# Optimization experiments

Hardware: AMD Instinct MI355X
Metric: run time of the kernel (lower is better)

The kernel has to match this reference:

```python
import jax, jax.numpy as jnp
import numpy as np

TEMP1 = 4.0  # self.temp1

def l2norm(x, eps=1e-8):
    # matches torch ref: x / (sqrt(sum(x^2)) + eps)
    return x / (jnp.sqrt(jnp.sum(x * x, axis=-1, keepdims=True)) + eps)

def setup_inputs() -> dict:
    key = jax.random.key(0)
    ks = jax.random.split(key, 8)
    B, C, H, W, D, Q = 32, 1024, 16, 16, 1000, 64
    return {
        "img_features_l": jax.random.normal(ks[0], (B, C, H, W), jnp.float32),
        "img_features_f": jax.random.normal(ks[1], (B, C, H, W), jnp.float32),
        "words_emb": jax.random.normal(ks[2], (B, D, Q), jnp.float32),
        "conv_w": jax.random.normal(ks[3], (D, C), jnp.float32) * 0.02,
        "conv_b": jnp.zeros((D,), jnp.float32),
        "sa_wl": jax.random.normal(ks[4], (D, D), jnp.float32) * 0.02,
        "sa_bl": jnp.zeros((D,), jnp.float32),
        "sa_wg": jax.random.normal(ks[5], (D, D), jnp.float32) * 0.02,
        "sa_bg": jnp.zeros((D,), jnp.float32),
        "sa_wc": jax.random.normal(ks[6], (D,), jnp.float32) * 0.05,
        "sa_bc": jnp.zeros((), jnp.float32),
        "cap_w": jax.random.normal(ks[7], (D,), jnp.float32) * 0.05,
        "cap_b": jnp.zeros((), jnp.float32),
    }

def reference(img_features_l, img_features_f, words_emb, conv_w, conv_b,
              sa_wl, sa_bl, sa_wg, sa_bg, sa_wc, sa_bc, cap_w, cap_b):
    B = img_features_f.shape[0]
    Bw = words_emb.shape[0]
    # 1x1 conv (1024 -> 1000), then flatten spatial and concat frontal+lateral
    f = jnp.einsum('oc,bchw->bohw', conv_w, img_features_f) + conv_b[None, :, None, None]
    l = jnp.einsum('oc,bchw->bohw', conv_w, img_features_l) + conv_b[None, :, None, None]
    img = jnp.concatenate([f.reshape(B, f.shape[1], -1),
                           l.reshape(B, l.shape[1], -1)], axis=2)  # [B, D, S]

    # attention_fn, vectorized over the per-word Python loop (axis i)
    # attn[i,b,s,q] = sum_d img[b,d,s] * words[i,d,q]
    logits = jnp.einsum('bds,idq->ibsq', img, words_emb)            # [Bw,B,S,Q]
    a1 = jax.nn.softmax(logits, axis=-1)                            # softmax over queryL
    a2 = jax.nn.softmax(jnp.swapaxes(a1, -1, -2) * TEMP1, axis=-1)  # [Bw,B,Q,S], softmax over sourceL
    # weightedContext (already transposed to [i,b,q,d])
    wctx = jnp.einsum('bds,ibqs->ibqd', img, a2)                    # [Bw,B,Q,D]

    word_t = jnp.swapaxes(words_emb, 1, 2)[:, None]                 # [Bw,1,Q,D]
    sim_loc = l2norm(wctx * word_t)                                 # [Bw,B,Q,D]
    sim_ave = jnp.mean(sim_loc, axis=2)                             # [Bw,B,D]

    # SA module (dropout in eval mode => identity)
    l_emb = jnp.tanh(jnp.einsum('ibqd,de->ibqe', sim_loc, sa_wl) + sa_bl)
    g_emb = jnp.tanh(jnp.einsum('ibd,de->ibe', sim_ave, sa_wg) + sa_bg)
    common = l_emb * g_emb[:, :, None, :]                           # [Bw,B,Q,D]
    w = jnp.einsum('ibqd,d->ibq', common, sa_wc) + sa_bc            # [Bw,B,Q]
    w = jax.nn.softmax(w, axis=-1)
    new_global = l2norm(jnp.einsum('ibq,ibqd->ibd', w, sim_loc))    # [Bw,B,D]
    sim = jax.nn.sigmoid(jnp.einsum('ibd,d->ib', new_global, cap_w) + cap_b)

    similarities_cap = sim.T                                        # [B, Bw]
    att_maps = a2[jnp.arange(Bw), jnp.arange(Bw)]                   # [Bw,Q,S] (attn[i] per word i)
    return similarities_cap, att_maps
```

## Files before the change

kernel.cpp:

```cpp
#include <hip/hip_runtime.h>
#include <cstdint>

typedef unsigned short u16;
typedef unsigned int   u32;
typedef __attribute__((ext_vector_type(8))) short bf16x8;
typedef __attribute__((ext_vector_type(4))) float f32x4;

#define D_DIM 1000
#define C_IN  1024
#define HW    256
#define S_DIM 512
#define Q_DIM 64

__device__ __forceinline__ u16 f2b(float x) {
    u32 u = __builtin_bit_cast(u32, x);
    u32 r = (u + 0x7FFFu + ((u >> 16) & 1u)) >> 16;
    return (u16)r;
}
__device__ __forceinline__ float b2f(u16 h) {
    u32 u = ((u32)h) << 16;
    return __builtin_bit_cast(float, u);
}
__device__ __forceinline__ float ftanh(float x) {
    float e = __expf(2.f * x);
    return 1.f - 2.f / (e + 1.f);
}

#define GLOAD(ldsptr, gptr) \
    __builtin_amdgcn_global_load_lds( \
        (const __attribute__((address_space(1))) unsigned int*)(gptr), \
        (__attribute__((address_space(3))) unsigned int*)(ldsptr), 16, 0, 0)

__global__ __launch_bounds__(256) void k_prepAll(
    const float* __restrict__ feat_l, const float* __restrict__ feat_f,
    const float* __restrict__ cw, const float* __restrict__ words,
    const float* __restrict__ wl,
    u16* __restrict__ fT_hi, u16* __restrict__ fT_lo,
    u16* __restrict__ cwh, u16* __restrict__ cwl,
    u16* __restrict__ wth, u16* __restrict__ wtl,
    u16* __restrict__ wlT)
{
    __shared__ char SH[18432] __attribute__((aligned(16)));
    const int bid = blockIdx.x;
    const int tid = threadIdx.x;

    if (bid < 4096) {
        float (*T)[65] = (float(*)[65])SH;
        int ct = bid & 15, ht = (bid >> 4) & 3, half_ = (bid >> 6) & 1, b = bid >> 7;
        const float* src = (half_ ? feat_l : feat_f) + (size_t)b * C_IN * HW;
        {
            int cl = tid >> 2, h16 = (tid & 3) * 16;
            const float* p = src + (size_t)(ct * 64 + cl) * 256 + ht * 64 + h16;
            #pragma unroll
            for (int j = 0; j < 4; j++) {
                float4 v = *(const float4*)(p + j * 4);
                T[h16 + j * 4 + 0][cl] = v.x;
                T[h16 + j * 4 + 1][cl] = v.y;
                T[h16 + j * 4 + 2][cl] = v.z;
                T[h16 + j * 4 + 3][cl] = v.w;
            }
        }
        __syncthreads();
        {
            int hl = tid >> 2, c16 = (tid & 3) * 16;
            int srow = b * 512 + half_ * 256 + ht * 64 + hl;
            bf16x8 vh[2], vlo[2];
            #pragma unroll
            for (int g = 0; g < 2; g++)
                #pragma unroll
                for (int j = 0; j < 8; j++) {
                    float x = T[hl][c16 + g * 8 + j];
                    u16 hh = f2b(x);
                    vh[g][j] = (short)hh;
                    vlo[g][j] = (short)f2b(x - b2f(hh));
                }
            size_t o = (size_t)srow * 1024 + ct * 64 + c16;
            *(bf16x8*)(fT_hi + o) = vh[0];
            *(bf16x8*)(fT_hi + o + 8) = vh[1];
            *(bf16x8*)(fT_lo + o) = vlo[0];
            *(bf16x8*)(fT_lo + o + 8) = vlo[1];
        }
    } else if (bid < 5120) {
        int d = bid - 4096;
        int c4 = tid * 4;
        ushort4 h = make_ushort4(0, 0, 0, 0), lo = make_ushort4(0, 0, 0, 0);
        if (d < D_DIM) {
            float4 v = *(const float4*)(cw + (size_t)d * 1024 + c4);
            float a[4] = {v.x, v.y, v.z, v.w};
            u16* ph = (u16*)&h; u16* pl = (u16*)&lo;
            #pragma unroll
            for (int j = 0; j < 4; j++) {
                ph[j] = f2b(a[j]);
                pl[j] = f2b(a[j] - b2f(ph[j]));
            }
        }
        *(ushort4*)(cwh + (size_t)d * 1024 + c4) = h;
        *(ushort4*)(cwl + (size_t)d * 1024 + c4) = lo;
    } else if (bid < 5632) {
        int lb = bid - 5120;
        int i = lb >> 4, dt = lb & 15;
        const float* src = words + (size_t)i * D_DIM * Q_DIM;
        u16 (*Th)[72] = (u16(*)[72])SH;
        u16 (*Tl)[72] = (u16(*)[72])(SH + 9216);
        #pragma unroll
        for (int rep = 0; rep < 4; rep++) {
            int idx = tid + rep * 256;
            int dl = idx >> 4, q4 = (idx & 15) * 4;
            int d = dt * 64 + dl;
            float4 v = make_float4(0.f, 0.f, 0.f, 0.f);
            if (d < D_DIM) v = *(const float4*)(src + (size_t)d * Q_DIM + q4);
            float a[4] = {v.x, v.y, v.z, v.w};
            #pragma unroll
            for (int jj = 0; jj < 4; jj++) {
                u16 hh = f2b(a[jj]);
                Th[dl][q4 + jj] = hh;
                Tl[dl][q4 + jj] = f2b(a[jj] - b2f(hh));
            }
        }
        __syncthreads();
        #pragma unroll
        for (int rep = 0; rep < 2; rep++) {
            int idx = tid + rep * 256;
            int q = idx >> 3, c8 = idx & 7;
            bf16x8 vh, vlo;
            #pragma unroll
            for (int jj = 0; jj < 8; jj++) { vh[jj] = (short)Th[c8 * 8 + jj][q]; vlo[jj] = (short)Tl[c8 * 8 + jj][q]; }
            size_t doff = (size_t)i * 65536 + (size_t)q * 1024 + dt * 64 + c8 * 8;
            *(bf16x8*)(wth + doff) = vh;
            *(bf16x8*)(wtl + doff) = vlo;
        }
    } else {
        int lb = bid - 5632;
        float (*t)[65] = (float(*)[65])SH;
        int bd = lb & 15, be = lb >> 4;
        int tx = tid & 15, ty = tid >> 4;
        #pragma unroll
        for (int rr = 0; rr < 4; rr++) {
            int r = ty * 4 + rr;
            int d = bd * 64 + r;
            int e4 = be * 64 + tx * 4;
            float v0 = 0.f, v1 = 0.f, v2 = 0.f, v3 = 0.f;
            if (d < D_DIM) {
                if (e4 + 3 < D_DIM) {
                    float4 v = *reinterpret_cast<const float4*>(wl + (size_t)d * D_DIM + e4);
                    v0 = v.x; v1 = v.y; v2 = v.z; v3 = v.w;
                } else {
                    if (e4 + 0 < D_DIM) v0 = wl[(size_t)d * D_DIM + e4 + 0];
                    if (e4 + 1 < D_DIM) v1 = wl[(size_t)d * D_DIM + e4 + 1];
                    if (e4 + 2 < D_DIM) v2 = wl[(size_t)d * D_DIM + e4 + 2];
                    if (e4 + 3 < D_DIM) v3 = wl[(size_t)d * D_DIM + e4 + 3];
                }
            }
            t[r][tx * 4 + 0] = v0; t[r][tx * 4 + 1] = v1;
            t[r][tx * 4 + 2] = v2; t[r][tx * 4 + 3] = v3;
        }
        __syncthreads();
        #pragma unroll
        for (int rr = 0; rr < 4; rr++) {
            int r2 = ty * 4 + rr;
            int e = be * 64 + r2;
            int d0 = bd * 64 + tx * 4;
            ushort4 h;
            h.x = f2b(t[tx * 4 + 0][r2]); h.y = f2b(t[tx * 4 + 1][r2]);
            h.z = f2b(t[tx * 4 + 2][r2]); h.w = f2b(t[tx * 4 + 3][r2]);
            *reinterpret_cast<ushort4*>(wlT + (size_t)e * 1024 + d0) = h;
        }
    }
}

__global__ __launch_bounds__(512) void k_convG(
    const u16* __restrict__ fT_hi, const u16* __restrict__ fT_lo,
    const u16* __restrict__ cwh, const u16* __restrict__ cwl,
    const float* __restrict__ cb,
    u16* __restrict__ img_hi, u16* __restrict__ imgT_hi, u16* __restrict__ imgT_lo)
{
    const int bid0 = blockIdx.x;
    const int bid = (bid0 & 7) * 32 + (bid0 >> 3);
    const int mblk = bid >> 2, nt = bid & 3;
    const int m0 = mblk * 256, n0 = nt * 256;

    __shared__ char LDS[131072] __attribute__((aligned(16)));
    __shared__ float cbS[256];

    const int tid = threadIdx.x;
    const int wid = tid >> 6, lane = tid & 63;
    const int wr = wid >> 2, wc = wid & 3;
    const int l15 = lane & 15, l4 = lane >> 4;
    const int sw = (l15 >> 1) & 3;

    if (tid < 256) {
        int d = n0 + tid;
        cbS[tid] = (d < D_DIM) ? cb[d] : 0.f;
    }

    auto stage = [&](int buf, int k0) {
        char* base = LDS + buf * 65536;
        #pragma unroll
        for (int rep = 0; rep < 2; rep++) {
            int idx = tid + rep * 512;
            int row = idx >> 2, slot = idx & 3;
            int kb = (slot ^ ((row >> 1) & 3)) * 16;
            size_t ao = (size_t)(m0 + row) * 2048 + (size_t)k0 * 2 + kb;
            size_t bo = (size_t)(n0 + row) * 2048 + (size_t)k0 * 2 + kb;
            GLOAD(base + idx * 16, (const char*)fT_hi + ao);
            GLOAD(base + 16384 + idx * 16, (const char*)fT_lo + ao);
            GLOAD(base + 32768 + idx * 16, (const char*)cwh + bo);
            GLOAD(base + 49152 + idx * 16, (const char*)cwl + bo);
        }
    };

    f32x4 acc[8][4] = {};

    stage(0, 0);
    __syncthreads();
    int cur = 0;
    for (int k0 = 0; k0 < 1024; k0 += 32) {
        if (k0 + 32 < 1024) stage(cur ^ 1, k0 + 32);
        const char* Ah = LDS + cur * 65536;
        const char* Alo = Ah + 16384;
        const char* Bh = Ah + 32768;
        const char* Blo = Ah + 49152;
        bf16x8 ah[8], bh[4];
        #pragma unroll
        for (int mf = 0; mf < 8; mf++)
            ah[mf] = *(const bf16x8*)(Ah + (wr * 128 + mf * 16 + l15) * 64 + ((l4 ^ sw) * 16));
        #pragma unroll
        for (int nf = 0; nf < 4; nf++)
            bh[nf] = *(const bf16x8*)(Bh + (wc * 64 + nf * 16 + l15) * 64 + ((l4 ^ sw) * 16));
        #pragma unroll
        for (int mf = 0; mf < 8; mf++)
            #pragma unroll
            for (int nf = 0; nf < 4; nf++)
                acc[mf][nf] = __builtin_amdgcn_mfma_f32_16x16x32_bf16(ah[mf], bh[nf], acc[mf][nf], 0, 0, 0);
        #pragma unroll
        for (int mf = 0; mf < 8; mf++) {
            bf16x8 al = *(const bf16x8*)(Alo + (wr * 128 + mf * 16 + l15) * 64 + ((l4 ^ sw) * 16));
            #pragma unroll
            for (int nf = 0; nf < 4; nf++)
                acc[mf][nf] = __builtin_amdgcn_mfma_f32_16x16x32_bf16(al, bh[nf], acc[mf][nf], 0, 0, 0);
        }
        #pragma unroll
        for (int nf = 0; nf < 4; nf++) {
            bf16x8 bl = *(const bf16x8*)(Blo + (wc * 64 + nf * 16 + l15) * 64 + ((l4 ^ sw) * 16));
            #pragma unroll
            for (int mf = 0; mf < 8; mf++)
                acc[mf][nf] = __builtin_amdgcn_mfma_f32_16x16x32_bf16(ah[mf], bl, acc[mf][nf], 0, 0, 0);
        }
        __syncthreads();
        cur ^= 1;
    }
    const int b = m0 >> 9;
    const int sbase = m0 & 511;
    #pragma unroll
    for (int mf = 0; mf < 8; mf++) {
        int srow = sbase + wr * 128 + mf * 16 + l4 * 4;
        #pragma unroll
        for (int nf = 0; nf < 4; nf++) {
            int dcol = n0 + wc * 64 + nf * 16 + l15;
            float bias = cbS[wc * 64 + nf * 16 + l15];
            ushort4 h4;
            u16* ph = (u16*)&h4;
            #pragma unroll
            for (int r = 0; r < 4; r++)
                ph[r] = f2b(acc[mf][nf][r] + bias);
            *(ushort4*)(img_hi + ((size_t)b * 1024 + dcol) * 512 + srow) = h4;
        }
    }
    u16* Thi = (u16*)LDS;
    u16* Tlo = (u16*)(LDS + 33792);
    #pragma unroll
    for (int qt = 0; qt < 4; qt++) {
        __syncthreads();
        if (wr == (qt >> 1)) {
            #pragma unroll
            for (int mm = 0; mm < 4; mm++) {
                int mf = (qt & 1) * 4 + mm;
                int sq = mm * 16 + l4 * 4;
                #pragma unroll
                for (int nf = 0; nf < 4; nf++) {
                    int dcol = wc * 64 + nf * 16 + l15;
                    float bias = cbS[dcol];
                    #pragma unroll
                    for (int r = 0; r < 4; r++) {
                        float v = acc[mf][nf][r] + bias;
                        u16 hh = f2b(v);
                        Thi[(sq + r) * 264 + dcol] = hh;
                        Tlo[(sq + r) * 264 + dcol] = f2b(v - b2f(hh));
                    }
                }
            }
        }
        __syncthreads();
        #pragma unroll
        for (int rep = 0; rep < 4; rep++) {
            int g = tid + rep * 512;
            int s = g >> 5, d8 = (g & 31) * 8;
            size_t go = ((size_t)b * 512 + sbase + qt * 64 + s) * 1024 + n0 + d8;
            *(bf16x8*)(imgT_hi + go) = *(const bf16x8*)(&Thi[s * 264 + d8]);
            *(bf16x8*)(imgT_lo + go) = *(const bf16x8*)(&Tlo[s * 264 + d8]);
        }
    }
}

__global__ __launch_bounds__(512) void k_logits(
    const u16* __restrict__ wTh, const u16* __restrict__ wTl,
    const u16* __restrict__ iTh, const u16* __restrict__ iTl,
    u16* __restrict__ U, float* __restrict__ Zp, float* __restrict__ out)
{
    const int bid0 = blockIdx.x;
    const int bid = (bid0 & 7) * 64 + (bid0 >> 3);
    const int b = bid >> 4, mt = (bid >> 1) & 7, nt = bid & 1;
    const int m0 = mt * 256, n0 = nt * 256;

    __shared__ char LDS[131072] __attribute__((aligned(16)));

    const int tid = threadIdx.x;
    const int wid = tid >> 6, lane = tid & 63;
    const int wr = wid >> 2, wc = wid & 3;
    const int l15 = lane & 15, l4 = lane >> 4;
    const int sw = (l15 >> 1) & 3;

    auto stage = [&](int buf, int k0) {
        char* base = LDS + buf * 65536;
        #pragma unroll
        for (int rep = 0; rep < 2; rep++) {
            int idx = tid + rep * 512;
            int row = idx >> 2, slot = idx & 3;
            int kb = (slot ^ ((row >> 1) & 3)) * 16;
            size_t ao = (size_t)(m0 + row) * 2048 + (size_t)k0 * 2 + kb;
            size_t bo = ((size_t)b * 512 + n0 + row) * 2048 + (size_t)k0 * 2 + kb;
            GLOAD(base + idx * 16, (const char*)wTh + ao);
            GLOAD(base + 16384 + idx * 16, (const char*)wTl + ao);
            GLOAD(base + 32768 + idx * 16, (const char*)iTh + bo);
            GLOAD(base + 49152 + idx * 16, (const char*)iTl + bo);
        }
    };

    f32x4 acc[8][4] = {};

    stage(0, 0);
    __syncthreads();
    int cur = 0;
    for (int k0 = 0; k0 < 1024; k0 += 32) {
        if (k0 + 32 < 1024) stage(cur ^ 1, k0 + 32);
        const char* Ah = LDS + cur * 65536;
        const char* Alo = Ah + 16384;
        const char* Bh = Ah + 32768;
        const char* Blo = Ah + 49152;
        bf16x8 ah[8], bh[4];
        #pragma unroll
        for (int mf = 0; mf < 8; mf++)
            ah[mf] = *(const bf16x8*)(Ah + (wr * 128 + mf * 16 + l15) * 64 + ((l4 ^ sw) * 16));
        #pragma unroll
        for (int nf = 0; nf < 4; nf++)
            bh[nf] = *(const bf16x8*)(Bh + (wc * 64 + nf * 16 + l15) * 64 + ((l4 ^ sw) * 16));
        #pragma unroll
        for (int mf = 0; mf < 8; mf++)
            #pragma unroll
            for (int nf = 0; nf < 4; nf++)
                acc[mf][nf] = __builtin_amdgcn_mfma_f32_16x16x32_bf16(ah[mf], bh[nf], acc[mf][nf], 0, 0, 0);
        #pragma unroll
        for (int mf = 0; mf < 8; mf++) {
            bf16x8 al = *(const bf16x8*)(Alo + (wr * 128 + mf * 16 + l15) * 64 + ((l4 ^ sw) * 16));
            #pragma unroll
            for (int nf = 0; nf < 4; nf++)
                acc[mf][nf] = __builtin_amdgcn_mfma_f32_16x16x32_bf16(al, bh[nf], acc[mf][nf], 0, 0, 0);
        }
        #pragma unroll
        for (int nf = 0; nf < 4; nf++) {
            bf16x8 bl = *(const bf16x8*)(Blo + (wc * 64 + nf * 16 + l15) * 64 + ((l4 ^ sw) * 16));
            #pragma unroll
            for (int mf = 0; mf < 8; mf++)
                acc[mf][nf] = __builtin_amdgcn_mfma_f32_16x16x32_bf16(ah[mf], bl, acc[mf][nf], 0, 0, 0);
        }
        __syncthreads();
        cur ^= 1;
    }

    float zacc[8][4] = {};
    #pragma unroll
    for (int il = 0; il < 2; il++) {
        int i_glob = mt * 4 + wr * 2 + il;
        bool diag = (i_glob == b);
        #pragma unroll
        for (int nf = 0; nf < 4; nf++) {
            int scol = n0 + wc * 64 + nf * 16 + l15;
            float m = -3.4e38f;
            #pragma unroll
            for (int mm = 0; mm < 4; mm++)
                #pragma unroll
                for (int r = 0; r < 4; r++)
                    m = fmaxf(m, acc[il * 4 + mm][nf][r]);
            m = fmaxf(m, __shfl_xor(m, 16));
            m = fmaxf(m, __shfl_xor(m, 32));
            float e[16], sum = 0.f;
            #pragma unroll
            for (int mm = 0; mm < 4; mm++)
                #pragma unroll
                for (int r = 0; r < 4; r++) {
                    float ev = __expf(acc[il * 4 + mm][nf][r] - m);
                    e[mm * 4 + r] = ev; sum += ev;
                }
            sum += __shfl_xor(sum, 16);
            sum += __shfl_xor(sum, 32);
            float inv = 1.f / sum;
            #pragma unroll
            for (int mm = 0; mm < 4; mm++)
                #pragma unroll
                for (int r = 0; r < 4; r++) {
                    float u = __expf(4.f * e[mm * 4 + r] * inv);
                    u16 ub = f2b(u);
                    zacc[il * 4 + mm][r] += b2f(ub);
                    int iqrow = m0 + wr * 128 + (il * 4 + mm) * 16 + l4 * 4 + r;
                    U[((size_t)b * 2048 + iqrow) * 512 + scol] = ub;
                    if (diag) {
                        int q = iqrow & 63;
                        out[1024 + ((size_t)i_glob * 64 + q) * 512 + scol] = u;
                    }
                }
        }
    }
    #pragma unroll
    for (int mf = 0; mf < 8; mf++)
        #pragma unroll
        for (int r = 0; r < 4; r++) {
            float z = zacc[mf][r];
            z += __shfl_xor(z, 1); z += __shfl_xor(z, 2);
            z += __shfl_xor(z, 4); z += __shfl_xor(z, 8);
            if (l15 == 0) {
                int iqrow = m0 + wr * 128 + mf * 16 + l4 * 4 + r;
                Zp[((size_t)b * 2048 + iqrow) * 8 + nt * 4 + wc] = z;
            }
        }
}

__global__ __launch_bounds__(256) void k_zat(
    const float* __restrict__ Zp, float* __restrict__ invZf, float* __restrict__ out)
{
    const int bid = blockIdx.x;
    const int tid = threadIdx.x;
    if (bid < 256) {
        int gi = bid * 256 + tid;
        float4 z0 = *(const float4*)(Zp + (size_t)gi * 8);
        float4 z1 = *(const float4*)(Zp + (size_t)gi * 8 + 4);
        invZf[gi] = 1.f / (z0.x + z0.y + z0.z + z0.w + z1.x + z1.y + z1.z + z1.w);
    } else {
        const int i = bid - 256;
        float* am = out + 1024 + (size_t)i * Q_DIM * S_DIM;
        int q = tid >> 2, ch = tid & 3;
        float s = 0.f;
        for (int ss = ch * 128; ss < ch * 128 + 128; ss++) s += am[(size_t)q * S_DIM + ss];
        s += __shfl_xor(s, 1);
        s += __shfl_xor(s, 2);
        float iz = 1.f / s;
        for (int ss = ch * 128; ss < ch * 128 + 128; ss++) am[(size_t)q * S_DIM + ss] *= iz;
    }
}

__global__ __launch_bounds__(512) void k_wctx(
    const u16* __restrict__ img_hi, const u16* __restrict__ U,
    const float* __restrict__ invZf,
    const u16* __restrict__ wTh, const u16* __restrict__ wTl,
    u16* __restrict__ vbuf, float* __restrict__ ssqp)
{
    const int bid0 = blockIdx.x;
    const int bid = (bid0 & 7) * 128 + (bid0 >> 3);
    const int b = bid >> 5, mt = (bid >> 3) & 3, nt = bid & 7;
    const int m0 = mt * 256, n0 = nt * 256;

    __shared__ char LDS[65536] __attribute__((aligned(16)));
    __shared__ float izS[256];

    const int tid = threadIdx.x;
    const int wid = tid >> 6, lane = tid & 63;
    const int wr = wid >> 2, wc = wid & 3;
    const int l15 = lane & 15, l4 = lane >> 4;
    const int sw = (l15 >> 1) & 3;

    if (tid < 256) izS[tid] = invZf[b * 2048 + n0 + tid];

    auto stage = [&](int buf, int k0) {
        char* base = LDS + buf * 32768;
        #pragma unroll
        for (int rep = 0; rep < 2; rep++) {
            int idx = tid + rep * 512;
            int row = idx >> 2, slot = idx & 3;
            int kb = (slot ^ ((row >> 1) & 3)) * 16;
            GLOAD(base + idx * 16, (const char*)img_hi + ((size_t)b * 1024 + m0 + row) * 1024 + (size_t)k0 * 2 + kb);
            GLOAD(base + 16384 + idx * 16, (const char*)U + ((size_t)b * 2048 + n0 + row) * 1024 + (size_t)k0 * 2 + kb);
        }
    };

    f32x4 acc[8][4] = {};

    stage(0, 0);
    __syncthreads();
    int cur = 0;
    for (int k0 = 0; k0 < 512; k0 += 32) {
        if (k0 + 32 < 512) stage(cur ^ 1, k0 + 32);
        const char* At = LDS + cur * 32768;
        const char* Bt = At + 16384;
        bf16x8 a[8], bb[4];
        #pragma unroll
        for (int mf = 0; mf < 8; mf++)
            a[mf] = *(const bf16x8*)(At + (wr * 128 + mf * 16 + l15) * 64 + ((l4 ^ sw) * 16));
        #pragma unroll
        for (int nf = 0; nf < 4; nf++)
            bb[nf] = *(const bf16x8*)(Bt + (wc * 64 + nf * 16 + l15) * 64 + ((l4 ^ sw) * 16));
        #pragma unroll
        for (int mf = 0; mf < 8; mf++)
            #pragma unroll
            for (int nf = 0; nf < 4; nf++)
                acc[mf][nf] = __builtin_amdgcn_mfma_f32_16x16x32_bf16(a[mf], bb[nf], acc[mf][nf], 0, 0, 0);
        __syncthreads();
        cur ^= 1;
    }

    #pragma unroll
    for (int nf = 0; nf < 4; nf++) {
        int col = wc * 64 + nf * 16 + l15;
        int iq = n0 + col;
        float iz = izS[col];
        size_t wtoff = (size_t)iq * 1024;
        float s_nf = 0.f;
        #pragma unroll
        for (int mf = 0; mf < 8; mf++) {
            int d0 = m0 + wr * 128 + mf * 16 + l4 * 4;
            ushort4 wh = *(const ushort4*)(wTh + wtoff + d0);
            ushort4 wl = *(const ushort4*)(wTl + wtoff + d0);
            const u16* pwh = (const u16*)&wh;
            const u16* pwl = (const u16*)&wl;
            ushort4 vo;
            u16* pv = (u16*)&vo;
            #pragma unroll
            for (int r = 0; r < 4; r++) {
                float wv = b2f(pwh[r]) + b2f(pwl[r]);
                float v = acc[mf][nf][r] * iz * wv;
                s_nf = fmaf(v, v, s_nf);
                pv[r] = f2b(v);
            }
            *(ushort4*)(vbuf + ((size_t)b * 2048 + iq) * 1024 + d0) = vo;
        }
        s_nf += __shfl_xor(s_nf, 16);
        s_nf += __shfl_xor(s_nf, 32);
        if (l4 == 0) ssqp[((size_t)b * 2048 + iq) * 4 + mt] = s_nf;
    }
}

__global__ __launch_bounds__(256) void k_postwg(
    const u16* __restrict__ vbuf, const float* __restrict__ ssqp,
    float* __restrict__ invn_ws, u16* __restrict__ simave_bf,
    const float* __restrict__ wg, u16* __restrict__ wgT)
{
    __shared__ char SH[16640] __attribute__((aligned(16)));
    const int bid = blockIdx.x;
    const int tid = threadIdx.x;

    if (bid < 1024) {
        const int pair = bid;
        float* invnS = (float*)SH;
        if (tid < 64) {
            size_t o = ((size_t)pair * 64 + tid) * 4;
            float s = ssqp[o] + ssqp[o + 1] + ssqp[o + 2] + ssqp[o + 3];
            float n = 1.f / (sqrtf(s) + 1e-8f);
            invnS[tid] = n;
            invn_ws[pair * 64 + tid] = n;
        }
        __syncthreads();
        int d0 = tid * 4;
        ushort4 o4 = make_ushort4(0, 0, 0, 0);
        if (d0 < D_DIM) {
            float a0 = 0.f, a1 = 0.f, a2 = 0.f, a3 = 0.f;
            const u16* vb = vbuf + (size_t)pair * 65536;
            for (int q = 0; q < 64; q++) {
                float n = invnS[q];
                ushort4 v = *(const ushort4*)(vb + q * 1024 + d0);
                a0 = fmaf(b2f(v.x), n, a0); a1 = fmaf(b2f(v.y), n, a1);
                a2 = fmaf(b2f(v.z), n, a2); a3 = fmaf(b2f(v.w), n, a3);
            }
            o4.x = f2b(a0 * (1.f / 64.f)); o4.y = f2b(a1 * (1.f / 64.f));
            o4.z = f2b(a2 * (1.f / 64.f)); o4.w = f2b(a3 * (1.f / 64.f));
        }
        *(ushort4*)(simave_bf + (size_t)pair * 1024 + d0) = o4;
    } else {
        int lb = bid - 1024;
        float (*t)[65] = (float(*)[65])SH;
        int bd = lb & 15, be = lb >> 4;
        int tx = tid & 15, ty = tid >> 4;
        #pragma unroll
        for (int rr = 0; rr < 4; rr++) {
            int r = ty * 4 + rr;
            int d = bd * 64 + r;
            int e4 = be * 64 + tx * 4;
            float v0 = 0.f, v1 = 0.f, v2 = 0.f, v3 = 0.f;
            if (d < D_DIM) {
                if (e4 + 3 < D_DIM) {
                    float4 v = *reinterpret_cast<const float4*>(wg + (size_t)d * D_DIM + e4);
                    v0 = v.x; v1 = v.y; v2 = v.z; v3 = v.w;
                } else {
                    if (e4 + 0 < D_DIM) v0 = wg[(size_t)d * D_DIM + e4 + 0];
                    if (e4 + 1 < D_DIM) v1 = wg[(size_t)d * D_DIM + e4 + 1];
                    if (e4 + 2 < D_DIM) v2 = wg[(size_t)d * D_DIM + e4 + 2];
                    if (e4 + 3 < D_DIM) v3 = wg[(size_t)d * D_DIM + e4 + 3];
                }
            }
            t[r][tx * 4 + 0] = v0; t[r][tx * 4 + 1] = v1;
            t[r][tx * 4 + 2] = v2; t[r][tx * 4 + 3] = v3;
        }
        __syncthreads();
        #pragma unroll
        for (int rr = 0; rr < 4; rr++) {
            int r2 = ty * 4 + rr;
            int e = be * 64 + r2;
            int d0 = bd * 64 + tx * 4;
            ushort4 h;
            h.x = f2b(t[tx * 4 + 0][r2]); h.y = f2b(t[tx * 4 + 1][r2]);
            h.z = f2b(t[tx * 4 + 2][r2]); h.w = f2b(t[tx * 4 + 3][r2]);
            *reinterpret_cast<ushort4*>(wgT + (size_t)e * 1024 + d0) = h;
        }
    }
}

__global__ __launch_bounds__(256) void k_g2M(
    const u16* __restrict__ simave_bf, const u16* __restrict__ wgT,
    const float* __restrict__ bg, const float* __restrict__ wc,
    float* __restrict__ g2)
{
    const int mt = blockIdx.x >> 3, nt = blockIdx.x & 7;
    const int m0 = mt * 128, n0 = nt * 128;

    __shared__ char LDS[65536] __attribute__((aligned(16)));
    __shared__ float bgS[128], wcS[128];

    const int tid = threadIdx.x;
    const int wid = tid >> 6, lane = tid & 63;
    const int wr = wid >> 1, wc_ = wid & 1;
    const int l15 = lane & 15, l4 = lane >> 4;
    const int sw = l15 & 7;

    if (tid < 128) {
        int e = n0 + tid;
        bgS[tid] = (e < D_DIM) ? bg[e] : 0.f;
        wcS[tid] = (e < D_DIM) ? wc[e] : 0.f;
    }

    auto stage = [&](int buf, int k0) {
        char* base = LDS + buf * 32768;
        #pragma unroll
        for (int rep = 0; rep < 4; rep++) {
            int idx = tid + rep * 256;
            int row = idx >> 3, slot = idx & 7;
            int kb = (slot ^ (row & 7)) * 16;
            GLOAD(base + idx * 16, (const char*)simave_bf + (size_t)(m0 + row) * 2048 + (size_t)k0 * 2 + kb);
            GLOAD(base + 16384 + idx * 16, (const char*)wgT + (size_t)(n0 + row) * 2048 + (size_t)k0 * 2 + kb);
        }
    };

    f32x4 acc[4][4] = {};

    stage(0, 0);
    __syncthreads();
    int cur = 0;
    for (int k0 = 0; k0 < 1024; k0 += 64) {
        if (k0 + 64 < 1024) stage(cur ^ 1, k0 + 64);
        const char* Al = LDS + cur * 32768;
        const char* Bl = Al + 16384;
        #pragma unroll
        for (int kf = 0; kf < 2; kf++) {
            bf16x8 a[4], bb[4];
            #pragma unroll
            for (int mf = 0; mf < 4; mf++)
                a[mf] = *(const bf16x8*)(Al + (wr * 64 + mf * 16 + l15) * 128 + (((kf * 4 + l4) ^ sw) * 16));
            #pragma unroll
            for (int nf = 0; nf < 4; nf++)
                bb[nf] = *(const bf16x8*)(Bl + (wc_ * 64 + nf * 16 + l15) * 128 + (((kf * 4 + l4) ^ sw) * 16));
            #pragma unroll
            for (int mf = 0; mf < 4; mf++)
                #pragma unroll
                for (int nf = 0; nf < 4; nf++)
                    acc[mf][nf] = __builtin_amdgcn_mfma_f32_16x16x32_bf16(a[mf], bb[nf], acc[mf][nf], 0, 0, 0);
        }
        __syncthreads();
        cur ^= 1;
    }

    #pragma unroll
    for (int mf = 0; mf < 4; mf++) {
        int p = m0 + wr * 64 + mf * 16 + l4 * 4;
        #pragma unroll
        for (int nf = 0; nf < 4; nf++) {
            int cl = wc_ * 64 + nf * 16 + l15;
            float bgv = bgS[cl], wcv = wcS[cl];
            #pragma unroll
            for (int r = 0; r < 4; r++)
                g2[(size_t)(p + r) * 1024 + n0 + cl] = ftanh(acc[mf][nf][r] + bgv) * wcv;
        }
    }
}

__global__ __launch_bounds__(512) void k_saG(
    const u16* __restrict__ vbuf, const u16* __restrict__ wlT,
    const float* __restrict__ invn_ws, const float* __restrict__ g2_ws,
    const float* __restrict__ bl, float* __restrict__ wspart)
{
    const int bid = blockIdx.x;
    const int wg = (bid & 7) * 128 + (bid >> 3);
    const int mt = wg >> 2, nt = wg & 3;
    const int m0 = mt * 256, n0 = nt * 256;

    __shared__ char LDS[65536] __attribute__((aligned(16)));
    __shared__ float invnS[256];
    __shared__ float blS[256];
    __shared__ float g2S[4 * 256];

    const int tid = threadIdx.x;
    const int wid = tid >> 6, lane = tid & 63;
    const int wr = wid >> 2, wc = wid & 3;
    const int l15 = lane & 15, l4 = lane >> 4;
    const int sw = (l15 >> 1) & 3;

    if (tid < 256) {
        invnS[tid] = invn_ws[m0 + tid];
        int e = n0 + tid;
        blS[tid] = (e < D_DIM) ? bl[e] : 0.f;
    }
    #pragma unroll
    for (int rep = 0; rep < 2; rep++) {
        int idx = tid + rep * 512;
        int p = idx >> 8, el = idx & 255;
        g2S[idx] = g2_ws[(size_t)((m0 >> 6) + p) * 1024 + n0 + el];
    }

    auto stage = [&](int buf, int k0) {
        char* base = LDS + buf * 32768;
        #pragma unroll
        for (int rep = 0; rep < 2; rep++) {
            int idx = tid + rep * 512;
            int row = idx >> 2, slot = idx & 3;
            int kb = (slot ^ ((row >> 1) & 3)) * 16;
            GLOAD(base + idx * 16, (const char*)vbuf + (size_t)(m0 + row) * 2048 + (size_t)k0 * 2 + kb);
            GLOAD(base + 16384 + idx * 16, (const char*)wlT + (size_t)(n0 + row) * 2048 + (size_t)k0 * 2 + kb);
        }
    };

    f32x4 acc[8][4] = {};

    stage(0, 0);
    __syncthreads();
    int cur = 0;
    for (int k0 = 0; k0 < 1024; k0 += 32) {
        if (k0 + 32 < 1024) stage(cur ^ 1, k0 + 32);
        const char* Al = LDS + cur * 32768;
        const char* Bl = Al + 16384;
        bf16x8 a[8], bb[4];
        #pragma unroll
        for (int mf = 0; mf < 8; mf++)
            a[mf] = *(const bf16x8*)(Al + (wr * 128 + mf * 16 + l15) * 64 + ((l4 ^ sw) * 16));
        #pragma unroll
        for (int nf = 0; nf < 4; nf++)
            bb[nf] = *(const bf16x8*)(Bl + (wc * 64 + nf * 16 + l15) * 64 + ((l4 ^ sw) * 16));
        #pragma unroll
        for (int mf = 0; mf < 8; mf++)
            #pragma unroll
            for (int nf = 0; nf < 4; nf++)
                acc[mf][nf] = __builtin_amdgcn_mfma_f32_16x16x32_bf16(a[mf], bb[nf], acc[mf][nf], 0, 0, 0);
        __syncthreads();
        cur ^= 1;
    }

    #pragma unroll
    for (int mf = 0; mf < 8; mf++) {
        int mrow = wr * 128 + mf * 16 + l4 * 4;
        #pragma unroll
        for (int r = 0; r < 4; r++) {
            float inv = invnS[mrow + r];
            int p = (mrow + r) >> 6;
            float s = 0.f;
            #pragma unroll
            for (int nf = 0; nf < 4; nf++) {
                int el = wc * 64 + nf * 16 + l15;
                float x = acc[mf][nf][r] * inv + blS[el];
                s += ftanh(x) * g2S[p * 256 + el];
            }
            s += __shfl_xor(s, 1);
            s += __shfl_xor(s, 2);
            s += __shfl_xor(s, 4);
            s += __shfl_xor(s, 8);
            if (l15 == 0)
                wspart[(size_t)(nt * 4 + wc) * 65536 + m0 + mrow + r] = s;
        }
    }
}

__global__ __launch_bounds__(256) void k_sa2(
    const float* __restrict__ wspart, const float* __restrict__ invn_ws,
    const u16* __restrict__ vbuf, const float* __restrict__ capw,
    const float* __restrict__ capb, float* __restrict__ out)
{
    const int pair = blockIdx.x;
    const u16* vb = vbuf + (size_t)pair * 65536;

    __shared__ float wiS[64];
    __shared__ float red[8];

    const int tid = threadIdx.x;

    if (tid < 64) {
        float x = 0.f;
        #pragma unroll
        for (int c = 0; c < 16; c++) x += wspart[(size_t)c * 65536 + pair * 64 + tid];
        float m = x;
        #pragma unroll
        for (int mk = 1; mk < 64; mk <<= 1) m = fmaxf(m, __shfl_xor(m, mk));
        float e = __expf(x - m);
        float Z = e;
        #pragma unroll
        for (int mk = 1; mk < 64; mk <<= 1) Z += __shfl_xor(Z, mk);
        wiS[tid] = (e / Z) * invn_ws[pair * 64 + tid];
    }
    __syncthreads();

    float s1 = 0.f, s2 = 0.f;
    int d0 = tid * 4;
    if (d0 < D_DIM) {
        float a0 = 0.f, a1 = 0.f, a2 = 0.f, a3 = 0.f;
        for (int q = 0; q < 64; q++) {
            float wq = wiS[q];
            ushort4 v = *(const ushort4*)(vb + q * 1024 + d0);
            a0 = fmaf(wq, b2f(v.x), a0); a1 = fmaf(wq, b2f(v.y), a1);
            a2 = fmaf(wq, b2f(v.z), a2); a3 = fmaf(wq, b2f(v.w), a3);
        }
        float4 cw4 = *(const float4*)(capw + d0);
        s1 = a0 * cw4.x + a1 * cw4.y + a2 * cw4.z + a3 * cw4.w;
        s2 = a0 * a0 + a1 * a1 + a2 * a2 + a3 * a3;
    }
    #pragma unroll
    for (int mk = 1; mk < 64; mk <<= 1) { s1 += __shfl_xor(s1, mk); s2 += __shfl_xor(s2, mk); }
    if ((tid & 63) == 0) { red[tid >> 6] = s1; red[4 + (tid >> 6)] = s2; }
    __syncthreads();
    if (tid == 0) {
        float S1 = red[0] + red[1] + red[2] + red[3];
        float S2 = red[4] + red[5] + red[6] + red[7];
        float val = S1 / (sqrtf(S2) + 1e-8f) + capb[0];
        out[pair] = 1.f / (1.f + __expf(-val));
    }
}

extern "C" void kernel_launch(void* const* d_in, const int* in_sizes, int n_in,
                              void* d_out, int out_size, void* d_ws, size_t ws_size,
                              hipStream_t stream)
{
    const float* feat_l = (const float*)d_in[0];
    const float* feat_f = (const float*)d_in[1];
    const float* words  = (const float*)d_in[2];
    const float* conv_w = (const float*)d_in[3];
    const float* conv_b = (const float*)d_in[4];
    const float* sa_wl  = (const float*)d_in[5];
    const float* sa_bl  = (const float*)d_in[6];
    const float* sa_wg  = (const float*)d_in[7];
    const float* sa_bg  = (const float*)d_in[8];
    const float* sa_wc  = (const float*)d_in[9];
    const float* cap_w  = (const float*)d_in[11];
    const float* cap_b  = (const float*)d_in[12];
    float* out = (float*)d_out;

    char* ws = (char*)d_ws;
    u16*   featT_hi  = (u16*)(ws);
    u16*   featT_lo  = (u16*)(ws + 33554432);
    u16*   imgT_hi   = (u16*)(ws + 67108864);
    u16*   imgT_lo   = (u16*)(ws + 100663296);
    u16*   vbuf      = (u16*)(ws);
    u16*   img_hi    = (u16*)(ws + 134217728);
    u16*   wgT       = (u16*)(ws + 134217728);
    u16*   U         = (u16*)(ws + 167772160);
    float* wspart    = (float*)(ws + 167772160);
    u16*   wT_hi     = (u16*)(ws + 234881024);
    u16*   simave_bf = (u16*)(ws + 234881024);
    u16*   wT_lo     = (u16*)(ws + 239075328);
    u16*   cw_hi     = (u16*)(ws + 243269632);
    float* Zp        = (float*)(ws + 243269632);
    u16*   cw_lo     = (u16*)(ws + 245366784);
    float* invZf     = (float*)(ws + 245366784);
    float* ssqp      = (float*)(ws + 245628928);
    float* invn      = (float*)(ws + 246677504);
    u16*   wlT       = (u16*)(ws + 247463936);
    float* g2        = (float*)(ws + 249561088);

    hipLaunchKernelGGL(k_prepAll, dim3(5888), dim3(256), 0, stream,
                       feat_l, feat_f, conv_w, words, sa_wl,
                       featT_hi, featT_lo, cw_hi, cw_lo, wT_hi, wT_lo, wlT);
    hipLaunchKernelGGL(k_convG, dim3(256), dim3(512), 0, stream,
                       featT_hi, featT_lo, cw_hi, cw_lo, conv_b,
                       img_hi, imgT_hi, imgT_lo);
    hipLaunchKernelGGL(k_logits, dim3(512), dim3(512), 0, stream,
                       wT_hi, wT_lo, imgT_hi, imgT_lo, U, Zp, out);
    hipLaunchKernelGGL(k_zat, dim3(288), dim3(256), 0, stream, Zp, invZf, out);
    hipLaunchKernelGGL(k_wctx, dim3(1024), dim3(512), 0, stream,
                       img_hi, U, invZf, wT_hi, wT_lo, vbuf, ssqp);
    hipLaunchKernelGGL(k_postwg, dim3(1280), dim3(256), 0, stream,
                       vbuf, ssqp, invn, simave_bf, sa_wg, wgT);
    hipLaunchKernelGGL(k_g2M, dim3(64), dim3(256), 0, stream,
                       simave_bf, wgT, sa_bg, sa_wc, g2);
    hipLaunchKernelGGL(k_saG, dim3(1024), dim3(512), 0, stream,
                       vbuf, wlT, invn, g2, sa_bl, wspart);
    hipLaunchKernelGGL(k_sa2, dim3(1024), dim3(256), 0, stream,
                       wspart, invn, vbuf, cap_w, cap_b, out);
}
```

Before: 677.5 us.

## Prefetch two stages ahead with partial vmcnt waits in GEMM main loops

Four MFMA GEMM loops are reworked to issue global-to-LDS loads two k-steps ahead. Each loop now uses s_waitcnt vmcnt(N) so it waits only for the older stage, where __syncthreads previously drained every outstanding load. Two raw s_barriers per iteration replace the single __syncthreads. The goal is to keep global loads in flight across the MFMA compute and hide memory latency better. The risks are an extra barrier per step and correctness that depends on the vmcnt counts matching the number of loads each stage issues.

Result: slower. 711.7 us (+5.0%).

```diff
diff --git a/kernel.cpp b/kernel.cpp
--- a/kernel.cpp
+++ b/kernel.cpp
@@ -30,6 +30,10 @@
     __builtin_amdgcn_global_load_lds( \
         (const __attribute__((address_space(1))) unsigned int*)(gptr), \
         (__attribute__((address_space(3))) unsigned int*)(ldsptr), 16, 0, 0)
+
+#define WAITV8()  do { asm volatile("s_waitcnt vmcnt(8)" ::: "memory"); __builtin_amdgcn_sched_barrier(0); } while (0)
+#define WAITV4()  do { asm volatile("s_waitcnt vmcnt(4)" ::: "memory"); __builtin_amdgcn_sched_barrier(0); } while (0)
+#define WAITV0()  do { asm volatile("s_waitcnt vmcnt(0)" ::: "memory"); __builtin_amdgcn_sched_barrier(0); } while (0)
 
 __global__ __launch_bounds__(256) void k_prepAll(
     const float* __restrict__ feat_l, const float* __restrict__ feat_f,
@@ -212,10 +216,11 @@
     f32x4 acc[8][4] = {};
 
     stage(0, 0);
-    __syncthreads();
-    int cur = 0;
-    for (int k0 = 0; k0 < 1024; k0 += 32) {
-        if (k0 + 32 < 1024) stage(cur ^ 1, k0 + 32);
+    stage(1, 32);
+    WAITV8();
+    __builtin_amdgcn_s_barrier();
+    for (int t = 0; t < 32; t++) {
+        const int cur = t & 1;
         const char* Ah = LDS + cur * 65536;
         const char* Alo = Ah + 16384;
         const char* Bh = Ah + 32768;
@@ -246,8 +251,14 @@
             for (int mf = 0; mf < 8; mf++)
                 acc[mf][nf] = __builtin_amdgcn_mfma_f32_16x16x32_bf16(ah[mf], bl, acc[mf][nf], 0, 0, 0);
         }
-        __syncthreads();
-        cur ^= 1;
+        __builtin_amdgcn_s_barrier();
+        if (t + 2 < 32) {
+            stage(cur, (t + 2) * 32);
+            WAITV8();
+        } else {
+            WAITV0();
+        }
+        __builtin_amdgcn_s_barrier();
     }
     const int b = m0 >> 9;
     const int sbase = m0 & 511;
@@ -339,10 +350,11 @@
     f32x4 acc[8][4] = {};
 
     stage(0, 0);
-    __syncthreads();
-    int cur = 0;
-    for (int k0 = 0; k0 < 1024; k0 += 32) {
-        if (k0 + 32 < 1024) stage(cur ^ 1, k0 + 32);
+    stage(1, 32);
+    WAITV8();
+    __builtin_amdgcn_s_barrier();
+    for (int t = 0; t < 32; t++) {
+        const int cur = t & 1;
         const char* Ah = LDS + cur * 65536;
         const char* Alo = Ah + 16384;
         const char* Bh = Ah + 32768;
@@ -373,8 +385,14 @@
             for (int mf = 0; mf < 8; mf++)
                 acc[mf][nf] = __builtin_amdgcn_mfma_f32_16x16x32_bf16(ah[mf], bl, acc[mf][nf], 0, 0, 0);
         }
-        __syncthreads();
-        cur ^= 1;
+        __builtin_amdgcn_s_barrier();
+        if (t + 2 < 32) {
+            stage(cur, (t + 2) * 32);
+            WAITV8();
+        } else {
+            WAITV0();
+        }
+        __builtin_amdgcn_s_barrier();
     }
 
     float zacc[8][4] = {};
@@ -494,10 +512,11 @@
     f32x4 acc[8][4] = {};
 
     stage(0, 0);
-    __syncthreads();
-    int cur = 0;
-    for (int k0 = 0; k0 < 512; k0 += 32) {
-        if (k0 + 32 < 512) stage(cur ^ 1, k0 + 32);
+    stage(1, 32);
+    WAITV4();
+    __builtin_amdgcn_s_barrier();
+    for (int t = 0; t < 16; t++) {
+        const int cur = t & 1;
         const char* At = LDS + cur * 32768;
         const char* Bt = At + 16384;
         bf16x8 a[8], bb[4];
@@ -512,8 +531,14 @@
             #pragma unroll
             for (int nf = 0; nf < 4; nf++)
                 acc[mf][nf] = __builtin_amdgcn_mfma_f32_16x16x32_bf16(a[mf], bb[nf], acc[mf][nf], 0, 0, 0);
-        __syncthreads();
-        cur ^= 1;
+        __builtin_amdgcn_s_barrier();
+        if (t + 2 < 16) {
+            stage(cur, (t + 2) * 32);
+            WAITV4();
+        } else {
+            WAITV0();
+        }
+        __builtin_amdgcn_s_barrier();
     }
 
     #pragma unroll
@@ -746,10 +771,11 @@
     f32x4 acc[8][4] = {};
 
     stage(0, 0);
-    __syncthreads();
-    int cur = 0;
-    for (int k0 = 0; k0 < 1024; k0 += 32) {
-        if (k0 + 32 < 1024) stage(cur ^ 1, k0 + 32);
+    stage(1, 32);
+    WAITV4();
+    __builtin_amdgcn_s_barrier();
+    for (int t = 0; t < 32; t++) {
+        const int cur = t & 1;
         const char* Al = LDS + cur * 32768;
         const char* Bl = Al + 16384;
         bf16x8 a[8], bb[4];
@@ -764,8 +790,14 @@
             #pragma unroll
             for (int nf = 0; nf < 4; nf++)
                 acc[mf][nf] = __builtin_amdgcn_mfma_f32_16x16x32_bf16(a[mf], bb[nf], acc[mf][nf], 0, 0, 0);
-        __syncthreads();
-        cur ^= 1;
+        __builtin_amdgcn_s_barrier();
+        if (t + 2 < 32) {
+            stage(cur, (t + 2) * 32);
+            WAITV4();
+        } else {
+            WAITV0();
+        }
+        __builtin_amdgcn_s_barrier();
     }
 
     #pragma unroll
```
